# Kernel tuning notes

Measured on AMD Instinct MI355X. Metric: run time of the kernel, lower is better.

## Reference

```python
import jax, jax.numpy as jnp
import numpy as np

REF_CHANNEL = 0
DIAG_EPS = 1e-7   # diag_loading coefficient
TIK_EPS = 1e-8    # additive eps in diagonal loading / trace denominator
MASK_EPS = 1e-15  # PSD mask-normalization eps


def _psd(spec, mask):
    # spec: (b, c, f, t) complex; mask: (b, f, t) real
    # PSD module: normalize mask over time, weight outer products, sum over t.
    m = mask / (mask.sum(axis=-1, keepdims=True) + MASK_EPS)
    return jnp.einsum('bcft,beft,bft->bfce', spec, spec.conj(), m.astype(spec.dtype))


def setup_inputs() -> dict:
    key = jax.random.key(0)
    k1, k2, k3, k4 = jax.random.split(key, 4)
    B, C, F, T = 4, 6, 257, 2000
    return {
        'spec_real': jax.random.normal(k1, (B, C, F, T), dtype=jnp.float32),
        'spec_imag': jax.random.normal(k2, (B, C, F, T), dtype=jnp.float32),
        'mask_s': jax.random.uniform(k3, (B, F, T), dtype=jnp.float32),
        'mask_n': jax.random.uniform(k4, (B, F, T), dtype=jnp.float32),
    }


def reference(spec_real, spec_imag, mask_s, mask_n):
    spec = spec_real + 1j * spec_imag                     # (b, c, f, t) complex64
    C = spec.shape[1]

    psd_s = _psd(spec, mask_s)                            # (b, f, c, c)
    psd_n = _psd(spec, mask_n)                            # (b, f, c, c)

    # Diagonal loading (Tikhonov regularization) of the noise PSD.
    tr_n = jnp.einsum('bfcc->bf', psd_n).real
    epsilon = jax.lax.stop_gradient(tr_n * DIAG_EPS + TIK_EPS)   # torch uses no_grad here
    psd_n = psd_n + epsilon[..., None, None] * jnp.eye(C, dtype=spec.dtype)

    # ref_channel solution: w = (psd_n^-1 psd_s) / trace(psd_n^-1 psd_s) @ u
    numerator = jnp.linalg.solve(psd_n, psd_s)            # (b, f, c, c)
    tr = jnp.einsum('bfcc->bf', numerator)
    ws = numerator / (tr[..., None, None] + TIK_EPS)
    w = ws[..., :, REF_CHANNEL]                           # one-hot u selects column -> (b, f, c)

    # enhanced = w^H Y
    enh = jnp.einsum('bfc,bcft->bft', w.conj(), spec)     # (b, f, t) complex
    return jnp.stack([enh.real, enh.imag], axis=-1)       # (b, f, t, 2) float32
```

## Files before the change

kernel.cpp:

```cpp
#include <hip/hip_runtime.h>

#define NB 4
#define NC 6
#define NF 257
#define NT 2000
#define NG (NB * NF)
#define NPAIR 15
#define NACC 74
#define NCHUNK 2
#define TCH (NT / NCHUNK)
#define NP4 (TCH / 4)
#define BLK 256
#define CS  (NF * NT)
#define CS4 (CS / 4)

typedef float nfloat4 __attribute__((ext_vector_type(4)));

__global__ __launch_bounds__(BLK) void psd_kernel(
    const float* __restrict__ sr, const float* __restrict__ si,
    const float* __restrict__ ms, const float* __restrict__ mn,
    float* __restrict__ wsp)
{
    constexpr int PC[NPAIR] = {0,0,0,0,0,1,1,1,1,2,2,2,3,3,4};
    constexpr int PE[NPAIR] = {1,2,3,4,5,2,3,4,5,3,4,5,4,5,5};

    const int bx = blockIdx.x;
    const int g  = bx >> 1;
    const int b  = g / NF;
    const int f  = g - b * NF;
    const int tb = (bx & 1) * TCH;
    const int sbase = b * NC * CS + f * NT + tb;
    const int mbase = g * NT + tb;

    const float4* s4r = (const float4*)(sr + sbase);
    const float4* s4i = (const float4*)(si + sbase);
    const float4* m4s = (const float4*)(ms + mbase);
    const float4* m4n = (const float4*)(mn + mbase);

    float acc[NACC];
    #pragma unroll
    for (int i = 0; i < NACC; i++) acc[i] = 0.f;

    const int p = threadIdx.x;
    if (p < NP4) {
        float wms[4], wmn[4], rr[NC][4], ii[NC][4];
        {
            const float4 t0 = m4s[p];
            wms[0] = t0.x; wms[1] = t0.y; wms[2] = t0.z; wms[3] = t0.w;
            const float4 t1 = m4n[p];
            wmn[0] = t1.x; wmn[1] = t1.y; wmn[2] = t1.z; wmn[3] = t1.w;
        }
        #pragma unroll
        for (int c = 0; c < NC; c++) {
            const float4 tr = s4r[c * CS4 + p];
            rr[c][0] = tr.x; rr[c][1] = tr.y; rr[c][2] = tr.z; rr[c][3] = tr.w;
            const float4 ti = s4i[c * CS4 + p];
            ii[c][0] = ti.x; ii[c][1] = ti.y; ii[c][2] = ti.z; ii[c][3] = ti.w;
        }
        acc[72] = wms[0] + wms[1] + wms[2] + wms[3];
        acc[73] = wmn[0] + wmn[1] + wmn[2] + wmn[3];
        #pragma unroll
        for (int c = 0; c < NC; c++) {
            #pragma unroll
            for (int k = 0; k < 4; k++) {
                const float d = rr[c][k] * rr[c][k] + ii[c][k] * ii[c][k];
                acc[c]     += d * wms[k];
                acc[6 + c] += d * wmn[k];
            }
        }
        #pragma unroll
        for (int q = 0; q < NPAIR; q++) {
            const int c = PC[q], e = PE[q];
            #pragma unroll
            for (int k = 0; k < 4; k++) {
                const float cr = rr[c][k] * rr[e][k] + ii[c][k] * ii[e][k];
                const float ci = ii[c][k] * rr[e][k] - rr[c][k] * ii[e][k];
                acc[12 + 4 * q + 0] += cr * wms[k];
                acc[12 + 4 * q + 1] += ci * wms[k];
                acc[12 + 4 * q + 2] += cr * wmn[k];
                acc[12 + 4 * q + 3] += ci * wmn[k];
            }
        }
    }

    #pragma unroll
    for (int i = 0; i < NACC; i++) {
        float v = acc[i];
        v += __shfl_down(v, 32);
        v += __shfl_down(v, 16);
        v += __shfl_down(v, 8);
        acc[i] = v;
    }

    __shared__ float red[32][NACC];
    const int wid  = threadIdx.x >> 6;
    const int lane = threadIdx.x & 63;
    if (lane < 8) {
        #pragma unroll
        for (int i = 0; i < NACC; i++) red[wid * 8 + lane][i] = acc[i];
    }
    __syncthreads();

    if (threadIdx.x < NACC) {
        float s = 0.f;
        #pragma unroll
        for (int r = 0; r < 32; r++) s += red[r][threadIdx.x];
        wsp[bx * NACC + threadIdx.x] = s;
    }
}

__global__ void solve_kernel(const float* __restrict__ wsp, float* __restrict__ wsw)
{
    const int gid = blockIdx.x * 64 + threadIdx.x;
    if (gid >= NG) return;

    constexpr int PC[NPAIR] = {0,0,0,0,0,1,1,1,1,2,2,2,3,3,4};
    constexpr int PE[NPAIR] = {1,2,3,4,5,2,3,4,5,3,4,5,4,5,5};

    const float* p0 = wsp + (2 * gid) * NACC;
    const float* p1 = p0 + NACC;
    float fin[NACC];
    #pragma unroll
    for (int i = 0; i < NACC; i++) fin[i] = p0[i] + p1[i];

    const float invS = 1.f / (fin[72] + 1e-15f);
    const float invN = 1.f / (fin[73] + 1e-15f);

    float Ar[NC][NC], Ai[NC][NC], Br[NC][NC], Bi[NC][NC];
    #pragma unroll
    for (int c = 0; c < NC; c++) {
        Br[c][c] = fin[c] * invS;     Bi[c][c] = 0.f;
        Ar[c][c] = fin[6 + c] * invN; Ai[c][c] = 0.f;
    }
    #pragma unroll
    for (int q = 0; q < NPAIR; q++) {
        const int c = PC[q], e = PE[q];
        const float sre = fin[12 + 4 * q + 0] * invS;
        const float sim = fin[12 + 4 * q + 1] * invS;
        const float nre = fin[12 + 4 * q + 2] * invN;
        const float nim = fin[12 + 4 * q + 3] * invN;
        Br[c][e] = sre;  Bi[c][e] = sim;
        Br[e][c] = sre;  Bi[e][c] = -sim;
        Ar[c][e] = nre;  Ai[c][e] = nim;
        Ar[e][c] = nre;  Ai[e][c] = -nim;
    }

    float trn = 0.f;
    #pragma unroll
    for (int c = 0; c < NC; c++) trn += Ar[c][c];
    const float eps = trn * 1e-7f + 1e-8f;
    #pragma unroll
    for (int c = 0; c < NC; c++) Ar[c][c] += eps;

    #pragma unroll
    for (int k = 0; k < NC; k++) {
        const float dr = Ar[k][k], di = Ai[k][k];
        const float idn = 1.f / (dr * dr + di * di);
        const float pr = dr * idn, pi = -di * idn;
        #pragma unroll
        for (int i2 = k + 1; i2 < NC; i2++) {
            const float fr = Ar[i2][k] * pr - Ai[i2][k] * pi;
            const float fi = Ar[i2][k] * pi + Ai[i2][k] * pr;
            #pragma unroll
            for (int j = k + 1; j < NC; j++) {
                Ar[i2][j] -= fr * Ar[k][j] - fi * Ai[k][j];
                Ai[i2][j] -= fr * Ai[k][j] + fi * Ar[k][j];
            }
            #pragma unroll
            for (int j = 0; j < NC; j++) {
                Br[i2][j] -= fr * Br[k][j] - fi * Bi[k][j];
                Bi[i2][j] -= fr * Bi[k][j] + fi * Br[k][j];
            }
        }
    }
    #pragma unroll
    for (int k = NC - 1; k >= 0; k--) {
        const float dr = Ar[k][k], di = Ai[k][k];
        const float idn = 1.f / (dr * dr + di * di);
        const float pr = dr * idn, pi = -di * idn;
        #pragma unroll
        for (int j = 0; j < NC; j++) {
            float xr = Br[k][j], xi = Bi[k][j];
            #pragma unroll
            for (int m = k + 1; m < NC; m++) {
                xr -= Ar[k][m] * Br[m][j] - Ai[k][m] * Bi[m][j];
                xi -= Ar[k][m] * Bi[m][j] + Ai[k][m] * Br[m][j];
            }
            Br[k][j] = xr * pr - xi * pi;
            Bi[k][j] = xr * pi + xi * pr;
        }
    }

    float trr = 1e-8f, tri = 0.f;
    #pragma unroll
    for (int c = 0; c < NC; c++) { trr += Br[c][c]; tri += Bi[c][c]; }
    const float idn = 1.f / (trr * trr + tri * tri);
    #pragma unroll
    for (int c = 0; c < NC; c++) {
        const float xr = Br[c][0], xi = Bi[c][0];
        const float wre = (xr * trr + xi * tri) * idn;
        const float wim = (xi * trr - xr * tri) * idn;
        wsw[gid * 12 + c]     = wre;
        wsw[gid * 12 + 6 + c] = -wim;
    }
}

__global__ __launch_bounds__(BLK) void apply_kernel(
    const float* __restrict__ sr, const float* __restrict__ si,
    const float* __restrict__ wsw, float* __restrict__ out)
{
    const int bx = blockIdx.x;
    const int g  = bx >> 1;
    const int b  = g / NF;
    const int f  = g - b * NF;
    const int tb = (bx & 1) * TCH;
    const int sbase = b * NC * CS + f * NT + tb;

    const float4* s4r = (const float4*)(sr + sbase);
    const float4* s4i = (const float4*)(si + sbase);

    float wr[NC], wi[NC];
    #pragma unroll
    for (int c = 0; c < NC; c++) {
        wr[c] = wsw[g * 12 + c];
        wi[c] = wsw[g * 12 + 6 + c];
    }

    nfloat4* o4 = (nfloat4*)(out + 2 * (g * NT + tb));

    const int p = threadIdx.x;
    if (p < NP4) {
        float rr[NC][4], ii[NC][4];
        #pragma unroll
        for (int c = 0; c < NC; c++) {
            const float4 tr = s4r[c * CS4 + p];
            rr[c][0] = tr.x; rr[c][1] = tr.y; rr[c][2] = tr.z; rr[c][3] = tr.w;
            const float4 ti = s4i[c * CS4 + p];
            ii[c][0] = ti.x; ii[c][1] = ti.y; ii[c][2] = ti.z; ii[c][3] = ti.w;
        }
        float er[4], ei[4];
        #pragma unroll
        for (int k = 0; k < 4; k++) {
            float a = 0.f, bb = 0.f;
            #pragma unroll
            for (int c = 0; c < NC; c++) {
                a  += wr[c] * rr[c][k] - wi[c] * ii[c][k];
                bb += wr[c] * ii[c][k] + wi[c] * rr[c][k];
            }
            er[k] = a; ei[k] = bb;
        }
        nfloat4 o0 = {er[0], ei[0], er[1], ei[1]};
        nfloat4 o1 = {er[2], ei[2], er[3], ei[3]};
        __builtin_nontemporal_store(o0, &o4[2 * p]);
        __builtin_nontemporal_store(o1, &o4[2 * p + 1]);
    }
}

extern "C" void kernel_launch(void* const* d_in, const int* in_sizes, int n_in,
                              void* d_out, int out_size, void* d_ws, size_t ws_size,
                              hipStream_t stream) {
    const float* sr = (const float*)d_in[0];
    const float* si = (const float*)d_in[1];
    const float* ms = (const float*)d_in[2];
    const float* mn = (const float*)d_in[3];
    float* out = (float*)d_out;

    float* wsp = (float*)d_ws;
    float* wsw = wsp + NG * NCHUNK * NACC;

    psd_kernel<<<NG * NCHUNK, BLK, 0, stream>>>(sr, si, ms, mn, wsp);
    solve_kernel<<<(NG + 63) / 64, 64, 0, stream>>>(wsp, wsw);
    apply_kernel<<<NG * NCHUNK, BLK, 0, stream>>>(sr, si, wsw, out);
}
```

Baseline: 179.3 us.

## Process full time axis per PSD block and restructure solve as LU with per-column substitution

The PSD kernel now uses one block per (batch, frequency) instead of two, and each thread accumulates two float4 time positions. This halves the partial-sum workspace and removes the two-partial merge in the solve kernel. The solve kernel stores the LU factors in place and solves the PSD_s right-hand sides one column at a time, keeping only column 0 and the trace, which lowers register pressure. It also gains launch_bounds(64,1). The trade-off is fewer PSD blocks (1028), which reduces parallelism for a bandwidth-bound pass, and longer serial work per thread.

```diff
diff --git a/kernel.cpp b/kernel.cpp
--- a/kernel.cpp
+++ b/kernel.cpp
@@ -7,30 +7,72 @@
 #define NG (NB * NF)
 #define NPAIR 15
 #define NACC 74
-#define NCHUNK 2
-#define TCH (NT / NCHUNK)
-#define NP4 (TCH / 4)
 #define BLK 256
 #define CS  (NF * NT)
 #define CS4 (CS / 4)
+#define NP4G (NT / 4)
+#define HALF4 (NP4G / 2)
 
 typedef float nfloat4 __attribute__((ext_vector_type(4)));
+
+__device__ __forceinline__ void psd_acc_pos(
+    const float4* __restrict__ s4r, const float4* __restrict__ s4i,
+    const float4* __restrict__ m4s, const float4* __restrict__ m4n,
+    int p, float (&acc)[NACC])
+{
+    constexpr int PC[NPAIR] = {0,0,0,0,0,1,1,1,1,2,2,2,3,3,4};
+    constexpr int PE[NPAIR] = {1,2,3,4,5,2,3,4,5,3,4,5,4,5,5};
+
+    float wms[4], wmn[4], rr[NC][4], ii[NC][4];
+    {
+        const float4 t0 = m4s[p];
+        wms[0] = t0.x; wms[1] = t0.y; wms[2] = t0.z; wms[3] = t0.w;
+        const float4 t1 = m4n[p];
+        wmn[0] = t1.x; wmn[1] = t1.y; wmn[2] = t1.z; wmn[3] = t1.w;
+    }
+    #pragma unroll
+    for (int c = 0; c < NC; c++) {
+        const float4 tr = s4r[c * CS4 + p];
+        rr[c][0] = tr.x; rr[c][1] = tr.y; rr[c][2] = tr.z; rr[c][3] = tr.w;
+        const float4 ti = s4i[c * CS4 + p];
+        ii[c][0] = ti.x; ii[c][1] = ti.y; ii[c][2] = ti.z; ii[c][3] = ti.w;
+    }
+    #pragma unroll
+    for (int k = 0; k < 4; k++) { acc[72] += wms[k]; acc[73] += wmn[k]; }
+    #pragma unroll
+    for (int c = 0; c < NC; c++) {
+        #pragma unroll
+        for (int k = 0; k < 4; k++) {
+            const float d = rr[c][k] * rr[c][k] + ii[c][k] * ii[c][k];
+            acc[c]     += d * wms[k];
+            acc[6 + c] += d * wmn[k];
+        }
+    }
+    #pragma unroll
+    for (int q = 0; q < NPAIR; q++) {
+        const int c = PC[q], e = PE[q];
+        #pragma unroll
+        for (int k = 0; k < 4; k++) {
+            const float cr = rr[c][k] * rr[e][k] + ii[c][k] * ii[e][k];
+            const float ci = ii[c][k] * rr[e][k] - rr[c][k] * ii[e][k];
+            acc[12 + 4 * q + 0] += cr * wms[k];
+            acc[12 + 4 * q + 1] += ci * wms[k];
+            acc[12 + 4 * q + 2] += cr * wmn[k];
+            acc[12 + 4 * q + 3] += ci * wmn[k];
+        }
+    }
+}
 
 __global__ __launch_bounds__(BLK) void psd_kernel(
     const float* __restrict__ sr, const float* __restrict__ si,
     const float* __restrict__ ms, const float* __restrict__ mn,
     float* __restrict__ wsp)
 {
-    constexpr int PC[NPAIR] = {0,0,0,0,0,1,1,1,1,2,2,2,3,3,4};
-    constexpr int PE[NPAIR] = {1,2,3,4,5,2,3,4,5,3,4,5,4,5,5};
-
-    const int bx = blockIdx.x;
-    const int g  = bx >> 1;
+    const int g  = blockIdx.x;
     const int b  = g / NF;
     const int f  = g - b * NF;
-    const int tb = (bx & 1) * TCH;
-    const int sbase = b * NC * CS + f * NT + tb;
-    const int mbase = g * NT + tb;
+    const int sbase = b * NC * CS + f * NT;
+    const int mbase = g * NT;
 
     const float4* s4r = (const float4*)(sr + sbase);
     const float4* s4i = (const float4*)(si + sbase);
@@ -42,45 +84,9 @@
     for (int i = 0; i < NACC; i++) acc[i] = 0.f;
 
     const int p = threadIdx.x;
-    if (p < NP4) {
-        float wms[4], wmn[4], rr[NC][4], ii[NC][4];
-        {
-            const float4 t0 = m4s[p];
-            wms[0] = t0.x; wms[1] = t0.y; wms[2] = t0.z; wms[3] = t0.w;
-            const float4 t1 = m4n[p];
-            wmn[0] = t1.x; wmn[1] = t1.y; wmn[2] = t1.z; wmn[3] = t1.w;
-        }
-        #pragma unroll
-        for (int c = 0; c < NC; c++) {
-            const float4 tr = s4r[c * CS4 + p];
-            rr[c][0] = tr.x; rr[c][1] = tr.y; rr[c][2] = tr.z; rr[c][3] = tr.w;
-            const float4 ti = s4i[c * CS4 + p];
-            ii[c][0] = ti.x; ii[c][1] = ti.y; ii[c][2] = ti.z; ii[c][3] = ti.w;
-        }
-        acc[72] = wms[0] + wms[1] + wms[2] + wms[3];
-        acc[73] = wmn[0] + wmn[1] + wmn[2] + wmn[3];
-        #pragma unroll
-        for (int c = 0; c < NC; c++) {
-            #pragma unroll
-            for (int k = 0; k < 4; k++) {
-                const float d = rr[c][k] * rr[c][k] + ii[c][k] * ii[c][k];
-                acc[c]     += d * wms[k];
-                acc[6 + c] += d * wmn[k];
-            }
-        }
-        #pragma unroll
-        for (int q = 0; q < NPAIR; q++) {
-            const int c = PC[q], e = PE[q];
-            #pragma unroll
-            for (int k = 0; k < 4; k++) {
-                const float cr = rr[c][k] * rr[e][k] + ii[c][k] * ii[e][k];
-                const float ci = ii[c][k] * rr[e][k] - rr[c][k] * ii[e][k];
-                acc[12 + 4 * q + 0] += cr * wms[k];
-                acc[12 + 4 * q + 1] += ci * wms[k];
-                acc[12 + 4 * q + 2] += cr * wmn[k];
-                acc[12 + 4 * q + 3] += ci * wmn[k];
-            }
-        }
+    if (p < HALF4) {
+        psd_acc_pos(s4r, s4i, m4s, m4n, p, acc);
+        psd_acc_pos(s4r, s4i, m4s, m4n, p + HALF4, acc);
     }
 
     #pragma unroll
@@ -105,52 +111,52 @@
         float s = 0.f;
         #pragma unroll
         for (int r = 0; r < 32; r++) s += red[r][threadIdx.x];
-        wsp[bx * NACC + threadIdx.x] = s;
-    }
-}
-
-__global__ void solve_kernel(const float* __restrict__ wsp, float* __restrict__ wsw)
+        wsp[g * NACC + threadIdx.x] = s;
+    }
+}
+
+__global__ __launch_bounds__(64, 1) void solve_kernel(
+    const float* __restrict__ wsp, float* __restrict__ wsw)
 {
     const int gid = blockIdx.x * 64 + threadIdx.x;
     if (gid >= NG) return;
 
     constexpr int PC[NPAIR] = {0,0,0,0,0,1,1,1,1,2,2,2,3,3,4};
     constexpr int PE[NPAIR] = {1,2,3,4,5,2,3,4,5,3,4,5,4,5,5};
-
-    const float* p0 = wsp + (2 * gid) * NACC;
-    const float* p1 = p0 + NACC;
+    constexpr int QIDX[NC][NC] = {
+        {-1, 0, 1, 2, 3, 4},
+        {-1,-1, 5, 6, 7, 8},
+        {-1,-1,-1, 9,10,11},
+        {-1,-1,-1,-1,12,13},
+        {-1,-1,-1,-1,-1,14},
+        {-1,-1,-1,-1,-1,-1}};
+
     float fin[NACC];
     #pragma unroll
-    for (int i = 0; i < NACC; i++) fin[i] = p0[i] + p1[i];
+    for (int i = 0; i < NACC; i++) fin[i] = wsp[gid * NACC + i];
 
     const float invS = 1.f / (fin[72] + 1e-15f);
     const float invN = 1.f / (fin[73] + 1e-15f);
 
-    float Ar[NC][NC], Ai[NC][NC], Br[NC][NC], Bi[NC][NC];
-    #pragma unroll
-    for (int c = 0; c < NC; c++) {
-        Br[c][c] = fin[c] * invS;     Bi[c][c] = 0.f;
-        Ar[c][c] = fin[6 + c] * invN; Ai[c][c] = 0.f;
-    }
+    float Ar[NC][NC], Ai[NC][NC];
+    #pragma unroll
+    for (int c = 0; c < NC; c++) { Ar[c][c] = fin[6 + c] * invN; Ai[c][c] = 0.f; }
     #pragma unroll
     for (int q = 0; q < NPAIR; q++) {
         const int c = PC[q], e = PE[q];
-        const float sre = fin[12 + 4 * q + 0] * invS;
-        const float sim = fin[12 + 4 * q + 1] * invS;
         const float nre = fin[12 + 4 * q + 2] * invN;
         const float nim = fin[12 + 4 * q + 3] * invN;
-        Br[c][e] = sre;  Bi[c][e] = sim;
-        Br[e][c] = sre;  Bi[e][c] = -sim;
         Ar[c][e] = nre;  Ai[c][e] = nim;
         Ar[e][c] = nre;  Ai[e][c] = -nim;
     }
-
-    float trn = 0.f;
-    #pragma unroll
-    for (int c = 0; c < NC; c++) trn += Ar[c][c];
-    const float eps = trn * 1e-7f + 1e-8f;
-    #pragma unroll
-    for (int c = 0; c < NC; c++) Ar[c][c] += eps;
+    {
+        float trn = 0.f;
+        #pragma unroll
+        for (int c = 0; c < NC; c++) trn += Ar[c][c];
+        const float eps = trn * 1e-7f + 1e-8f;
+        #pragma unroll
+        for (int c = 0; c < NC; c++) Ar[c][c] += eps;
+    }
 
     #pragma unroll
     for (int k = 0; k < NC; k++) {
@@ -158,48 +164,65 @@
         const float idn = 1.f / (dr * dr + di * di);
         const float pr = dr * idn, pi = -di * idn;
         #pragma unroll
-        for (int i2 = k + 1; i2 < NC; i2++) {
-            const float fr = Ar[i2][k] * pr - Ai[i2][k] * pi;
-            const float fi = Ar[i2][k] * pi + Ai[i2][k] * pr;
+        for (int i = k + 1; i < NC; i++) {
+            const float lr = Ar[i][k] * pr - Ai[i][k] * pi;
+            const float li = Ar[i][k] * pi + Ai[i][k] * pr;
+            Ar[i][k] = lr; Ai[i][k] = li;
             #pragma unroll
             for (int j = k + 1; j < NC; j++) {
-                Ar[i2][j] -= fr * Ar[k][j] - fi * Ai[k][j];
-                Ai[i2][j] -= fr * Ai[k][j] + fi * Ar[k][j];
-            }
-            #pragma unroll
-            for (int j = 0; j < NC; j++) {
-                Br[i2][j] -= fr * Br[k][j] - fi * Bi[k][j];
-                Bi[i2][j] -= fr * Bi[k][j] + fi * Br[k][j];
-            }
-        }
-    }
-    #pragma unroll
-    for (int k = NC - 1; k >= 0; k--) {
-        const float dr = Ar[k][k], di = Ai[k][k];
-        const float idn = 1.f / (dr * dr + di * di);
-        const float pr = dr * idn, pi = -di * idn;
-        #pragma unroll
-        for (int j = 0; j < NC; j++) {
-            float xr = Br[k][j], xi = Bi[k][j];
-            #pragma unroll
-            for (int m = k + 1; m < NC; m++) {
-                xr -= Ar[k][m] * Br[m][j] - Ai[k][m] * Bi[m][j];
-                xi -= Ar[k][m] * Bi[m][j] + Ai[k][m] * Br[m][j];
-            }
-            Br[k][j] = xr * pr - xi * pi;
-            Bi[k][j] = xr * pi + xi * pr;
+                Ar[i][j] -= lr * Ar[k][j] - li * Ai[k][j];
+                Ai[i][j] -= lr * Ai[k][j] + li * Ar[k][j];
+            }
         }
     }
 
     float trr = 1e-8f, tri = 0.f;
-    #pragma unroll
-    for (int c = 0; c < NC; c++) { trr += Br[c][c]; tri += Bi[c][c]; }
+    float w0r[NC], w0i[NC];
+    #pragma unroll
+    for (int j = 0; j < NC; j++) {
+        float xr[NC], xi[NC];
+        #pragma unroll
+        for (int i = 0; i < NC; i++) {
+            if (i == j)      { xr[i] = fin[j] * invS;                      xi[i] = 0.f; }
+            else if (i < j)  { const int q = QIDX[i][j];
+                               xr[i] = fin[12 + 4 * q] * invS;  xi[i] =  fin[13 + 4 * q] * invS; }
+            else             { const int q = QIDX[j][i];
+                               xr[i] = fin[12 + 4 * q] * invS;  xi[i] = -fin[13 + 4 * q] * invS; }
+        }
+        #pragma unroll
+        for (int i = 1; i < NC; i++) {
+            #pragma unroll
+            for (int k = 0; k < NC - 1; k++) if (k < i) {
+                xr[i] -= Ar[i][k] * xr[k] - Ai[i][k] * xi[k];
+                xi[i] -= Ar[i][k] * xi[k] + Ai[i][k] * xr[k];
+            }
+        }
+        #pragma unroll
+        for (int i = NC - 1; i >= 0; i--) {
+            #pragma unroll
+            for (int k = 0; k < NC; k++) if (k > i) {
+                xr[i] -= Ar[i][k] * xr[k] - Ai[i][k] * xi[k];
+                xi[i] -= Ar[i][k] * xi[k] + Ai[i][k] * xr[k];
+            }
+            const float dr = Ar[i][i], di = Ai[i][i];
+            const float idn = 1.f / (dr * dr + di * di);
+            const float pr = dr * idn, pi = -di * idn;
+            const float tr0 = xr[i] * pr - xi[i] * pi;
+            xi[i] = xr[i] * pi + xi[i] * pr;
+            xr[i] = tr0;
+        }
+        trr += xr[j]; tri += xi[j];
+        if (j == 0) {
+            #pragma unroll
+            for (int i = 0; i < NC; i++) { w0r[i] = xr[i]; w0i[i] = xi[i]; }
+        }
+    }
+
     const float idn = 1.f / (trr * trr + tri * tri);
     #pragma unroll
     for (int c = 0; c < NC; c++) {
-        const float xr = Br[c][0], xi = Bi[c][0];
-        const float wre = (xr * trr + xi * tri) * idn;
-        const float wim = (xi * trr - xr * tri) * idn;
+        const float wre = (w0r[c] * trr + w0i[c] * tri) * idn;
+        const float wim = (w0i[c] * trr - w0r[c] * tri) * idn;
         wsw[gid * 12 + c]     = wre;
         wsw[gid * 12 + 6 + c] = -wim;
     }
@@ -213,7 +236,7 @@
     const int g  = bx >> 1;
     const int b  = g / NF;
     const int f  = g - b * NF;
-    const int tb = (bx & 1) * TCH;
+    const int tb = (bx & 1) * (NT / 2);
     const int sbase = b * NC * CS + f * NT + tb;
 
     const float4* s4r = (const float4*)(sr + sbase);
@@ -229,7 +252,7 @@
     nfloat4* o4 = (nfloat4*)(out + 2 * (g * NT + tb));
 
     const int p = threadIdx.x;
-    if (p < NP4) {
+    if (p < HALF4) {
         float rr[NC][4], ii[NC][4];
         #pragma unroll
         for (int c = 0; c < NC; c++) {
@@ -266,9 +289,9 @@
     float* out = (float*)d_out;
 
     float* wsp = (float*)d_ws;
-    float* wsw = wsp + NG * NCHUNK * NACC;
-
-    psd_kernel<<<NG * NCHUNK, BLK, 0, stream>>>(sr, si, ms, mn, wsp);
+    float* wsw = wsp + NG * NACC;
+
+    psd_kernel<<<NG, BLK, 0, stream>>>(sr, si, ms, mn, wsp);
     solve_kernel<<<(NG + 63) / 64, 64, 0, stream>>>(wsp, wsw);
-    apply_kernel<<<NG * NCHUNK, BLK, 0, stream>>>(sr, si, wsw, out);
-}
+    apply_kernel<<<NG * 2, BLK, 0, stream>>>(sr, si, wsw, out);
+}
```

Measured after the change: 176.0 us. Within noise of the previous version (-1.8%).
